# Kernel optimization log

Hardware: AMD Instinct MI355X
Metric: run time of the kernel (lower is better)

The kernel has to match this reference:

```python
import jax, jax.numpy as jnp
import numpy as np

NEG_INF = -1e30  # stand-in for float('-inf') that is fp16/bf16-safe


def setup_inputs() -> dict:
    key = jax.random.key(0)
    ks = jax.random.split(key, 6)
    B, S, D, E = 4, 4096, 2048, 64
    return {
        "x": jax.random.normal(ks[0], (B, S, D), dtype=jnp.float32),
        "router_w": jax.random.normal(ks[1], (E, D), dtype=jnp.float32) * (1.0 / np.sqrt(D)),
        "router_b": jax.random.normal(ks[2], (E,), dtype=jnp.float32) * 0.01,
        "noise_w": jax.random.normal(ks[3], (E, D), dtype=jnp.float32) * (1.0 / np.sqrt(D)),
        "noise_b": jax.random.normal(ks[4], (E,), dtype=jnp.float32) * 0.01,
        "noise_u": jax.random.uniform(ks[5], (B, S, E), dtype=jnp.float32),
        "top_k": 2,
    }


def reference(x, router_w, router_b, noise_w, noise_b, noise_u, top_k):
    E = router_w.shape[0]
    # dual linear projections: [B,S,D] x [D,E] -> [B,S,E]
    logits = jnp.einsum("bsd,ed->bse", x, router_w) + router_b
    noise_scale = jax.nn.softplus(jnp.einsum("bsd,ed->bse", x, noise_w) + noise_b)
    noisy = logits + noise_scale * noise_u  # noise_u plays role of torch.rand_like
    # top-k over experts
    max_k, max_k_index = jax.lax.top_k(noisy, top_k)  # [B,S,k]
    # scatter top-k values into -inf-filled tensor == keep noisy at topk slots
    keep = jnp.sum(jax.nn.one_hot(max_k_index, E, dtype=noisy.dtype), axis=-2) > 0  # [B,S,E]
    sparse = jnp.where(keep, noisy, NEG_INF)
    sf_sparse_topk = jax.nn.softmax(sparse, axis=-1)
    return (sf_sparse_topk, max_k_index)
```

## Files before the change

### kernel.cpp

```cpp
#include <hip/hip_runtime.h>
#include <math.h>

typedef __fp16   fp16x2  __attribute__((ext_vector_type(2)));
typedef _Float16 half8   __attribute__((ext_vector_type(8)));
typedef float    floatx4 __attribute__((ext_vector_type(4)));

#define M_TOTAL 16384
#define K_DIM   2048
#define NCOL    128
#define BM      32
#define BK      32
#define NT      256
#define NCHUNK  (K_DIM / BK)

#define A_HI  0
#define A_LO  1024
#define B_HI  2048
#define B_LO  6144
#define BUF_H 10240

__device__ __forceinline__ void gl_lds16(const _Float16* g, _Float16* l) {
    __builtin_amdgcn_global_load_lds((const __attribute__((address_space(1))) void*)g,
                                     (__attribute__((address_space(3))) void*)l, 16, 0, 0);
}

__device__ __forceinline__ void cvt_store(const float4 v, _Float16* hiP, _Float16* loP) {
    fp16x2 h01 = __builtin_amdgcn_cvt_pkrtz(v.x, v.y);
    fp16x2 h23 = __builtin_amdgcn_cvt_pkrtz(v.z, v.w);
    float r0 = (v.x - (float)h01.x) * 2048.0f;
    float r1 = (v.y - (float)h01.y) * 2048.0f;
    float r2 = (v.z - (float)h23.x) * 2048.0f;
    float r3 = (v.w - (float)h23.y) * 2048.0f;
    fp16x2 l01 = __builtin_amdgcn_cvt_pkrtz(r0, r1);
    fp16x2 l23 = __builtin_amdgcn_cvt_pkrtz(r2, r3);
    union { fp16x2 h[2]; uint2 u; } ph, pl;
    ph.h[0] = h01; ph.h[1] = h23;
    pl.h[0] = l01; pl.h[1] = l23;
    *(uint2*)hiP = ph.u;
    *(uint2*)loP = pl.u;
}

__global__ __launch_bounds__(256) void conv_w_kernel(
    const float* __restrict__ rw, const float* __restrict__ nw,
    _Float16* __restrict__ wsB)
{
    const int u   = blockIdx.x * 256 + threadIdx.x;
    const int col = u & 127;
    const int g   = (u >> 7) & 3;
    const int c   = u >> 9;
    const float* srcRow = (col < 64) ? (rw + (size_t)col * K_DIM)
                                     : (nw + (size_t)(col - 64) * K_DIM);
    const float* src = srcRow + c * BK + g * 8;
    const float4 v0 = *(const float4*)src;
    const float4 v1 = *(const float4*)(src + 4);
    union { fp16x2 h[4]; uint4 q; } ph, pl;
    ph.h[0] = __builtin_amdgcn_cvt_pkrtz(v0.x, v0.y);
    ph.h[1] = __builtin_amdgcn_cvt_pkrtz(v0.z, v0.w);
    ph.h[2] = __builtin_amdgcn_cvt_pkrtz(v1.x, v1.y);
    ph.h[3] = __builtin_amdgcn_cvt_pkrtz(v1.z, v1.w);
    pl.h[0] = __builtin_amdgcn_cvt_pkrtz((v0.x - (float)ph.h[0].x) * 2048.0f,
                                         (v0.y - (float)ph.h[0].y) * 2048.0f);
    pl.h[1] = __builtin_amdgcn_cvt_pkrtz((v0.z - (float)ph.h[1].x) * 2048.0f,
                                         (v0.w - (float)ph.h[1].y) * 2048.0f);
    pl.h[2] = __builtin_amdgcn_cvt_pkrtz((v1.x - (float)ph.h[2].x) * 2048.0f,
                                         (v1.y - (float)ph.h[2].y) * 2048.0f);
    pl.h[3] = __builtin_amdgcn_cvt_pkrtz((v1.z - (float)ph.h[3].x) * 2048.0f,
                                         (v1.w - (float)ph.h[3].y) * 2048.0f);
    const size_t base = (size_t)c * 8192 + ((size_t)g * 128 + col) * 8;
    *(uint4*)&wsB[base]        = ph.q;
    *(uint4*)&wsB[base + 4096] = pl.q;
}

__global__ __launch_bounds__(NT, 2) void gemm_router_kernel(
    const float* __restrict__ x,
    const _Float16* __restrict__ wsB,
    const float* __restrict__ router_b,
    const float* __restrict__ noise_b,
    const float* __restrict__ noise_u,
    float* __restrict__ out)
{
    __shared__ __align__(16) union {
        _Float16 S[2 * BUF_H];
        struct { float Cs[32][132]; float p1[32]; float p2[32]; int i1[32]; int i2[32]; } e;
    } sm;

    const int t    = threadIdx.x;
    const int lane = t & 63;
    const int w    = t >> 6;
    const int rowBase = blockIdx.x * BM;

    const int r = t >> 3, q = t & 7;
    const float* pa = x + (size_t)(rowBase + r) * K_DIM + q * 4;
    const int aw = ((q >> 1) * 32 + r) * 8 + (q & 1) * 4;

    const int lr  = lane & 15;
    const int lg4 = lane >> 4;
    const int mt0 = (w & 1) * 16;
    const int nt0 = (w >> 1) * 64;
    const int aOff = (lg4 * 32 + mt0 + lr) * 8;

    floatx4 acch[4], accx[4];
    #pragma unroll
    for (int ni = 0; ni < 4; ++ni) { acch[ni] = (floatx4)0.0f; accx[ni] = (floatx4)0.0f; }

    float4 aReg = *(const float4*)pa;
    {
        #pragma unroll
        for (int i = 0; i < 4; ++i) {
            const int n = w * 4 + i;
            gl_lds16(wsB + n * 512 + lane * 8, &sm.S[B_HI + n * 512]);
        }
    }
    cvt_store(aReg, &sm.S[A_HI + aw], &sm.S[A_LO + aw]);

    for (int c = 0; c < NCHUNK; ++c) {
        __syncthreads();
        _Float16* buf  = sm.S + (c & 1) * BUF_H;
        _Float16* bufn = sm.S + ((c + 1) & 1) * BUF_H;

        if (c + 1 < NCHUNK) {
            const _Float16* wc = wsB + (size_t)(c + 1) * 8192;
            #pragma unroll
            for (int i = 0; i < 4; ++i) {
                const int n = w * 4 + i;
                gl_lds16(wc + n * 512 + lane * 8, bufn + B_HI + n * 512);
            }
            aReg = *(const float4*)(pa + (c + 1) * BK);
        }

        const half8 ah = *(const half8*)&buf[A_HI + aOff];
        const half8 al = *(const half8*)&buf[A_LO + aOff];
        half8 bh[4], bl[4];
        #pragma unroll
        for (int ni = 0; ni < 4; ++ni) {
            const int bo = (lg4 * 128 + nt0 + ni * 16 + lr) * 8;
            bh[ni] = *(const half8*)&buf[B_HI + bo];
            bl[ni] = *(const half8*)&buf[B_LO + bo];
        }
        #pragma unroll
        for (int ni = 0; ni < 4; ++ni) {
            acch[ni] = __builtin_amdgcn_mfma_f32_16x16x32_f16(ah, bh[ni], acch[ni], 0, 0, 0);
            accx[ni] = __builtin_amdgcn_mfma_f32_16x16x32_f16(ah, bl[ni], accx[ni], 0, 0, 0);
            accx[ni] = __builtin_amdgcn_mfma_f32_16x16x32_f16(al, bh[ni], accx[ni], 0, 0, 0);
        }
        if (c + 1 < NCHUNK)
            cvt_store(aReg, &bufn[A_HI + aw], &bufn[A_LO + aw]);
    }

    #pragma unroll
    for (int ni = 0; ni < 4; ++ni) {
        const floatx4 v = acch[ni] + accx[ni] * (1.0f / 2048.0f);
        const int col = nt0 + ni * 16 + lr;
        #pragma unroll
        for (int reg = 0; reg < 4; ++reg)
            sm.e.Cs[mt0 + lg4 * 4 + reg][col] = v[reg];
    }
    __syncthreads();

    {
        const int sr = t >> 3;
        const int eg = (t & 7) * 8;
        const int grow = rowBase + sr;
        const float* urow = noise_u + (size_t)grow * 64 + eg;
        const float4 u0 = *(const float4*)urow;
        const float4 u1 = *(const float4*)(urow + 4);
        const float uu[8] = {u0.x, u0.y, u0.z, u0.w, u1.x, u1.y, u1.z, u1.w};
        float v1 = -3.0e38f, v2 = -3.0e38f;
        int i1 = 0, i2 = 0;
        #pragma unroll
        for (int j = 0; j < 8; ++j) {
            const int e = eg + j;
            const float lg = sm.e.Cs[sr][e] + router_b[e];
            const float nz = sm.e.Cs[sr][64 + e] + noise_b[e];
            const float sp = fmaxf(nz, 0.0f) + log1pf(expf(-fabsf(nz)));
            const float nv = lg + sp * uu[j];
            if (nv > v1)      { v2 = v1; i2 = i1; v1 = nv; i1 = e; }
            else if (nv > v2) { v2 = nv; i2 = e; }
        }
        #pragma unroll
        for (int m = 1; m < 8; m <<= 1) {
            const float ov1 = __shfl_xor(v1, m, 64);
            const int   oi1 = __shfl_xor(i1, m, 64);
            const float ov2 = __shfl_xor(v2, m, 64);
            const int   oi2 = __shfl_xor(i2, m, 64);
            const bool takeO = (ov1 > v1) || (ov1 == v1 && oi1 < i1);
            const float t1v = takeO ? ov1 : v1;  const int t1i = takeO ? oi1 : i1;
            const float c2v = takeO ? v1 : ov1;  const int c2i = takeO ? i1 : oi1;
            const float c3v = takeO ? ov2 : v2;  const int c3i = takeO ? oi2 : i2;
            const bool k2 = (c3v > c2v) || (c3v == c2v && c3i < c2i);
            v1 = t1v; i1 = t1i;
            v2 = k2 ? c3v : c2v; i2 = k2 ? c3i : c2i;
        }
        if ((t & 7) == 0) {
            const float e2 = expf(v2 - v1);
            const float dn = 1.0f + e2;
            sm.e.p1[sr] = 1.0f / dn;
            sm.e.p2[sr] = e2 / dn;
            sm.e.i1[sr] = i1;
            sm.e.i2[sr] = i2;
            float2 idx2;
            idx2.x = (float)i1;
            idx2.y = (float)i2;
            *(float2*)&out[(size_t)M_TOTAL * 64 + (size_t)grow * 2] = idx2;
        }
    }
    __syncthreads();

    {
        const int rr = t >> 3;
        const int e0 = (t & 7) * 8;
        const int g2 = rowBase + rr;
        const int j1 = sm.e.i1[rr], j2 = sm.e.i2[rr];
        const float q1 = sm.e.p1[rr], q2 = sm.e.p2[rr];
        float* orow = out + (size_t)g2 * 64;
        #pragma unroll
        for (int g = 0; g < 2; ++g) {
            const int b0 = e0 + g * 4;
            float4 v;
            v.x = (b0 + 0 == j1) ? q1 : (b0 + 0 == j2) ? q2 : 0.0f;
            v.y = (b0 + 1 == j1) ? q1 : (b0 + 1 == j2) ? q2 : 0.0f;
            v.z = (b0 + 2 == j1) ? q1 : (b0 + 2 == j2) ? q2 : 0.0f;
            v.w = (b0 + 3 == j1) ? q1 : (b0 + 3 == j2) ? q2 : 0.0f;
            *(float4*)&orow[b0] = v;
        }
    }
}

extern "C" void kernel_launch(void* const* d_in, const int* in_sizes, int n_in,
                              void* d_out, int out_size, void* d_ws, size_t ws_size,
                              hipStream_t stream) {
    const float* x  = (const float*)d_in[0];
    const float* rw = (const float*)d_in[1];
    const float* rb = (const float*)d_in[2];
    const float* nw = (const float*)d_in[3];
    const float* nb = (const float*)d_in[4];
    const float* nu = (const float*)d_in[5];
    float* out = (float*)d_out;
    _Float16* wsB = (_Float16*)d_ws;
    (void)in_sizes; (void)n_in; (void)out_size; (void)ws_size;

    hipLaunchKernelGGL(conv_w_kernel, dim3(128), dim3(256), 0, stream, rw, nw, wsB);
    hipLaunchKernelGGL(gemm_router_kernel, dim3(M_TOTAL / BM), dim3(NT), 0, stream,
                       x, wsB, rb, nb, nu, out);
}
```

Before: 239.7 us.

## Load A fragments directly to registers and make B LDS staging per-wave, barrier-free

Result: slower. 265.1 us (+10.6%).

```diff
diff --git a/kernel.cpp b/kernel.cpp
--- a/kernel.cpp
+++ b/kernel.cpp
@@ -7,37 +7,14 @@
 
 #define M_TOTAL 16384
 #define K_DIM   2048
-#define NCOL    128
 #define BM      32
 #define BK      32
 #define NT      256
 #define NCHUNK  (K_DIM / BK)
 
-#define A_HI  0
-#define A_LO  1024
-#define B_HI  2048
-#define B_LO  6144
-#define BUF_H 10240
-
 __device__ __forceinline__ void gl_lds16(const _Float16* g, _Float16* l) {
     __builtin_amdgcn_global_load_lds((const __attribute__((address_space(1))) void*)g,
                                      (__attribute__((address_space(3))) void*)l, 16, 0, 0);
-}
-
-__device__ __forceinline__ void cvt_store(const float4 v, _Float16* hiP, _Float16* loP) {
-    fp16x2 h01 = __builtin_amdgcn_cvt_pkrtz(v.x, v.y);
-    fp16x2 h23 = __builtin_amdgcn_cvt_pkrtz(v.z, v.w);
-    float r0 = (v.x - (float)h01.x) * 2048.0f;
-    float r1 = (v.y - (float)h01.y) * 2048.0f;
-    float r2 = (v.z - (float)h23.x) * 2048.0f;
-    float r3 = (v.w - (float)h23.y) * 2048.0f;
-    fp16x2 l01 = __builtin_amdgcn_cvt_pkrtz(r0, r1);
-    fp16x2 l23 = __builtin_amdgcn_cvt_pkrtz(r2, r3);
-    union { fp16x2 h[2]; uint2 u; } ph, pl;
-    ph.h[0] = h01; ph.h[1] = h23;
-    pl.h[0] = l01; pl.h[1] = l23;
-    *(uint2*)hiP = ph.u;
-    *(uint2*)loP = pl.u;
 }
 
 __global__ __launch_bounds__(256) void conv_w_kernel(
@@ -80,7 +57,7 @@
     float* __restrict__ out)
 {
     __shared__ __align__(16) union {
-        _Float16 S[2 * BUF_H];
+        _Float16 B[2][4][4096];
         struct { float Cs[32][132]; float p1[32]; float p2[32]; int i1[32]; int i2[32]; } e;
     } sm;
 
@@ -89,63 +66,87 @@
     const int w    = t >> 6;
     const int rowBase = blockIdx.x * BM;
 
-    const int r = t >> 3, q = t & 7;
-    const float* pa = x + (size_t)(rowBase + r) * K_DIM + q * 4;
-    const int aw = ((q >> 1) * 32 + r) * 8 + (q & 1) * 4;
-
     const int lr  = lane & 15;
     const int lg4 = lane >> 4;
     const int mt0 = (w & 1) * 16;
     const int nt0 = (w >> 1) * 64;
-    const int aOff = (lg4 * 32 + mt0 + lr) * 8;
+
+    const float* pa = x + (size_t)(rowBase + mt0 + lr) * K_DIM + lg4 * 8;
+    const _Float16* wsrc = wsB + (size_t)nt0 * 8 + (size_t)lane * 8;
+
+    _Float16* const b0 = &sm.B[0][w][0];
+    _Float16* const b1 = &sm.B[1][w][0];
+
+    #pragma unroll
+    for (int g = 0; g < 4; ++g) {
+        gl_lds16(wsrc + g * 1024,        b0 + g * 512);
+        gl_lds16(wsrc + 4096 + g * 1024, b0 + 2048 + g * 512);
+    }
+    float4 A0a = *(const float4*)(pa);
+    float4 A0b = *(const float4*)(pa + 4);
+    float4 A1a = *(const float4*)(pa + 32);
+    float4 A1b = *(const float4*)(pa + 36);
 
     floatx4 acch[4], accx[4];
     #pragma unroll
     for (int ni = 0; ni < 4; ++ni) { acch[ni] = (floatx4)0.0f; accx[ni] = (floatx4)0.0f; }
 
-    float4 aReg = *(const float4*)pa;
-    {
-        #pragma unroll
-        for (int i = 0; i < 4; ++i) {
-            const int n = w * 4 + i;
-            gl_lds16(wsB + n * 512 + lane * 8, &sm.S[B_HI + n * 512]);
-        }
-    }
-    cvt_store(aReg, &sm.S[A_HI + aw], &sm.S[A_LO + aw]);
-
+    #pragma unroll 2
     for (int c = 0; c < NCHUNK; ++c) {
-        __syncthreads();
-        _Float16* buf  = sm.S + (c & 1) * BUF_H;
-        _Float16* bufn = sm.S + ((c + 1) & 1) * BUF_H;
-
-        if (c + 1 < NCHUNK) {
-            const _Float16* wc = wsB + (size_t)(c + 1) * 8192;
-            #pragma unroll
-            for (int i = 0; i < 4; ++i) {
-                const int n = w * 4 + i;
-                gl_lds16(wc + n * 512 + lane * 8, bufn + B_HI + n * 512);
-            }
-            aReg = *(const float4*)(pa + (c + 1) * BK);
-        }
-
-        const half8 ah = *(const half8*)&buf[A_HI + aOff];
-        const half8 al = *(const half8*)&buf[A_LO + aOff];
+        _Float16* const cur = (c & 1) ? b1 : b0;
+        _Float16* const nxt = (c & 1) ? b0 : b1;
+
+        const int cn  = (c + 1 < NCHUNK) ? c + 1 : NCHUNK - 1;
+        const int cn2 = (c + 2 < NCHUNK) ? c + 2 : NCHUNK - 1;
+        const _Float16* wsn = wsrc + (size_t)cn * 8192;
+        #pragma unroll
+        for (int g = 0; g < 4; ++g) {
+            gl_lds16(wsn + g * 1024,        nxt + g * 512);
+            gl_lds16(wsn + 4096 + g * 1024, nxt + 2048 + g * 512);
+        }
+        const float4 A2a = *(const float4*)(pa + cn2 * 32);
+        const float4 A2b = *(const float4*)(pa + cn2 * 32 + 4);
+
+        asm volatile("s_waitcnt vmcnt(10)" ::: "memory");
+
         half8 bh[4], bl[4];
         #pragma unroll
         for (int ni = 0; ni < 4; ++ni) {
-            const int bo = (lg4 * 128 + nt0 + ni * 16 + lr) * 8;
-            bh[ni] = *(const half8*)&buf[B_HI + bo];
-            bl[ni] = *(const half8*)&buf[B_LO + bo];
-        }
+            const int co = lg4 * 512 + (ni * 16 + lr) * 8;
+            bh[ni] = *(const half8*)&cur[co];
+            bl[ni] = *(const half8*)&cur[2048 + co];
+        }
+
+        union { fp16x2 h[4]; half8 v; } H, L;
+        H.h[0] = __builtin_amdgcn_cvt_pkrtz(A0a.x, A0a.y);
+        H.h[1] = __builtin_amdgcn_cvt_pkrtz(A0a.z, A0a.w);
+        H.h[2] = __builtin_amdgcn_cvt_pkrtz(A0b.x, A0b.y);
+        H.h[3] = __builtin_amdgcn_cvt_pkrtz(A0b.z, A0b.w);
+        L.h[0] = __builtin_amdgcn_cvt_pkrtz((A0a.x - (float)H.h[0].x) * 2048.0f,
+                                            (A0a.y - (float)H.h[0].y) * 2048.0f);
+        L.h[1] = __builtin_amdgcn_cvt_pkrtz((A0a.z - (float)H.h[1].x) * 2048.0f,
+                                            (A0a.w - (float)H.h[1].y) * 2048.0f);
+        L.h[2] = __builtin_amdgcn_cvt_pkrtz((A0b.x - (float)H.h[2].x) * 2048.0f,
+                                            (A0b.y - (float)H.h[2].y) * 2048.0f);
+        L.h[3] = __builtin_amdgcn_cvt_pkrtz((A0b.z - (float)H.h[3].x) * 2048.0f,
+                                            (A0b.w - (float)H.h[3].y) * 2048.0f);
+        const half8 ah = H.v;
+        const half8 al = L.v;
+
+        __builtin_amdgcn_s_setprio(1);
         #pragma unroll
         for (int ni = 0; ni < 4; ++ni) {
             acch[ni] = __builtin_amdgcn_mfma_f32_16x16x32_f16(ah, bh[ni], acch[ni], 0, 0, 0);
             accx[ni] = __builtin_amdgcn_mfma_f32_16x16x32_f16(ah, bl[ni], accx[ni], 0, 0, 0);
             accx[ni] = __builtin_amdgcn_mfma_f32_16x16x32_f16(al, bh[ni], accx[ni], 0, 0, 0);
         }
-        if (c + 1 < NCHUNK)
-            cvt_store(aReg, &bufn[A_HI + aw], &bufn[A_LO + aw]);
-    }
+        __builtin_amdgcn_s_setprio(0);
+
+        A0a = A1a; A0b = A1b; A1a = A2a; A1b = A2b;
+    }
+
+    asm volatile("s_waitcnt vmcnt(0)" ::: "memory");
+    __syncthreads();
 
     #pragma unroll
     for (int ni = 0; ni < 4; ++ni) {
@@ -215,13 +216,13 @@
         float* orow = out + (size_t)g2 * 64;
         #pragma unroll
         for (int g = 0; g < 2; ++g) {
-            const int b0 = e0 + g * 4;
+            const int b0i = e0 + g * 4;
             float4 v;
-            v.x = (b0 + 0 == j1) ? q1 : (b0 + 0 == j2) ? q2 : 0.0f;
-            v.y = (b0 + 1 == j1) ? q1 : (b0 + 1 == j2) ? q2 : 0.0f;
-            v.z = (b0 + 2 == j1) ? q1 : (b0 + 2 == j2) ? q2 : 0.0f;
-            v.w = (b0 + 3 == j1) ? q1 : (b0 + 3 == j2) ? q2 : 0.0f;
-            *(float4*)&orow[b0] = v;
+            v.x = (b0i + 0 == j1) ? q1 : (b0i + 0 == j2) ? q2 : 0.0f;
+            v.y = (b0i + 1 == j1) ? q1 : (b0i + 1 == j2) ? q2 : 0.0f;
+            v.z = (b0i + 2 == j1) ? q1 : (b0i + 2 == j2) ? q2 : 0.0f;
+            v.w = (b0i + 3 == j1) ? q1 : (b0i + 3 == j2) ? q2 : 0.0f;
+            *(float4*)&orow[b0i] = v;
         }
     }
 }
```

## Triple-buffer LDS and deepen prefetch pipeline with manual waitcnt barriers

Applied to the files above, without the earlier changes.

Result: faster. 230.9 us (-3.7%).

```diff
diff --git a/kernel.cpp b/kernel.cpp
--- a/kernel.cpp
+++ b/kernel.cpp
@@ -80,7 +80,7 @@
     float* __restrict__ out)
 {
     __shared__ __align__(16) union {
-        _Float16 S[2 * BUF_H];
+        _Float16 S[3 * BUF_H];
         struct { float Cs[32][132]; float p1[32]; float p2[32]; int i1[32]; int i2[32]; } e;
     } sm;
 
@@ -103,49 +103,75 @@
     #pragma unroll
     for (int ni = 0; ni < 4; ++ni) { acch[ni] = (floatx4)0.0f; accx[ni] = (floatx4)0.0f; }
 
-    float4 aReg = *(const float4*)pa;
-    {
-        #pragma unroll
-        for (int i = 0; i < 4; ++i) {
-            const int n = w * 4 + i;
-            gl_lds16(wsB + n * 512 + lane * 8, &sm.S[B_HI + n * 512]);
-        }
-    }
-    cvt_store(aReg, &sm.S[A_HI + aw], &sm.S[A_LO + aw]);
+    _Float16* p0 = sm.S;
+    _Float16* p1 = sm.S + BUF_H;
+    _Float16* p2 = sm.S + 2 * BUF_H;
+
+    float4 a0v = *(const float4*)pa;
+    float4 a1v = *(const float4*)(pa + BK);
+    asm volatile("" ::: "memory");
+    float4 aS = *(const float4*)(pa + 2 * BK);
+    #pragma unroll
+    for (int i = 0; i < 4; ++i) {
+        const int n = w * 4 + i;
+        gl_lds16(wsB + n * 512 + lane * 8, p0 + B_HI + n * 512);
+    }
+    asm volatile("" ::: "memory");
+    float4 aN = *(const float4*)(pa + 3 * BK);
+    #pragma unroll
+    for (int i = 0; i < 4; ++i) {
+        const int n = w * 4 + i;
+        gl_lds16(wsB + 8192 + n * 512 + lane * 8, p1 + B_HI + n * 512);
+    }
+    asm volatile("" ::: "memory");
+    asm volatile("s_waitcnt vmcnt(10)" ::: "memory");
+    cvt_store(a0v, &p0[A_HI + aw], &p0[A_LO + aw]);
+    cvt_store(a1v, &p1[A_HI + aw], &p1[A_LO + aw]);
+    asm volatile("s_waitcnt lgkmcnt(0)" ::: "memory");
 
     for (int c = 0; c < NCHUNK; ++c) {
-        __syncthreads();
-        _Float16* buf  = sm.S + (c & 1) * BUF_H;
-        _Float16* bufn = sm.S + ((c + 1) & 1) * BUF_H;
-
-        if (c + 1 < NCHUNK) {
-            const _Float16* wc = wsB + (size_t)(c + 1) * 8192;
+        asm volatile("s_waitcnt vmcnt(5)" ::: "memory");
+        asm volatile("s_barrier" ::: "memory");
+
+        const int cn2 = (c + 2 < NCHUNK) ? c + 2 : NCHUNK - 1;
+        const int cn4 = (c + 4 < NCHUNK) ? c + 4 : NCHUNK - 1;
+        float4 aNew = *(const float4*)(pa + cn4 * BK);
+        {
+            const _Float16* wc = wsB + (size_t)cn2 * 8192;
             #pragma unroll
             for (int i = 0; i < 4; ++i) {
                 const int n = w * 4 + i;
-                gl_lds16(wc + n * 512 + lane * 8, bufn + B_HI + n * 512);
+                gl_lds16(wc + n * 512 + lane * 8, p2 + B_HI + n * 512);
             }
-            aReg = *(const float4*)(pa + (c + 1) * BK);
-        }
-
-        const half8 ah = *(const half8*)&buf[A_HI + aOff];
-        const half8 al = *(const half8*)&buf[A_LO + aOff];
+        }
+
+        const half8 ah = *(const half8*)&p0[A_HI + aOff];
+        const half8 al = *(const half8*)&p0[A_LO + aOff];
         half8 bh[4], bl[4];
         #pragma unroll
         for (int ni = 0; ni < 4; ++ni) {
             const int bo = (lg4 * 128 + nt0 + ni * 16 + lr) * 8;
-            bh[ni] = *(const half8*)&buf[B_HI + bo];
-            bl[ni] = *(const half8*)&buf[B_LO + bo];
-        }
+            bh[ni] = *(const half8*)&p0[B_HI + bo];
+            bl[ni] = *(const half8*)&p0[B_LO + bo];
+        }
+
+        __builtin_amdgcn_s_setprio(1);
         #pragma unroll
         for (int ni = 0; ni < 4; ++ni) {
             acch[ni] = __builtin_amdgcn_mfma_f32_16x16x32_f16(ah, bh[ni], acch[ni], 0, 0, 0);
             accx[ni] = __builtin_amdgcn_mfma_f32_16x16x32_f16(ah, bl[ni], accx[ni], 0, 0, 0);
             accx[ni] = __builtin_amdgcn_mfma_f32_16x16x32_f16(al, bh[ni], accx[ni], 0, 0, 0);
         }
-        if (c + 1 < NCHUNK)
-            cvt_store(aReg, &bufn[A_HI + aw], &bufn[A_LO + aw]);
-    }
+        __builtin_amdgcn_s_setprio(0);
+
+        cvt_store(aS, &p2[A_HI + aw], &p2[A_LO + aw]);
+        aS = aN; aN = aNew;
+
+        _Float16* tmp = p0; p0 = p1; p1 = p2; p2 = tmp;
+    }
+
+    asm volatile("s_waitcnt vmcnt(0)" ::: "memory");
+    __syncthreads();
 
     #pragma unroll
     for (int ni = 0; ni < 4; ++ni) {
```

## Halve GEMM row tile to 16 rows and retarget occupancy to four blocks per CU

Applied to the files above, without the earlier changes.

New measurement: 256.0 us. +6.8%, slower.

```diff
diff --git a/kernel.cpp b/kernel.cpp
--- a/kernel.cpp
+++ b/kernel.cpp
@@ -8,36 +8,31 @@
 #define M_TOTAL 16384
 #define K_DIM   2048
 #define NCOL    128
-#define BM      32
+#define BM      16
 #define BK      32
 #define NT      256
 #define NCHUNK  (K_DIM / BK)
 
 #define A_HI  0
-#define A_LO  1024
-#define B_HI  2048
-#define B_LO  6144
-#define BUF_H 10240
+#define A_LO  512
+#define B_HI  1024
+#define B_LO  5120
+#define BUF_H 9216
 
 __device__ __forceinline__ void gl_lds16(const _Float16* g, _Float16* l) {
     __builtin_amdgcn_global_load_lds((const __attribute__((address_space(1))) void*)g,
                                      (__attribute__((address_space(3))) void*)l, 16, 0, 0);
 }
 
-__device__ __forceinline__ void cvt_store(const float4 v, _Float16* hiP, _Float16* loP) {
-    fp16x2 h01 = __builtin_amdgcn_cvt_pkrtz(v.x, v.y);
-    fp16x2 h23 = __builtin_amdgcn_cvt_pkrtz(v.z, v.w);
-    float r0 = (v.x - (float)h01.x) * 2048.0f;
-    float r1 = (v.y - (float)h01.y) * 2048.0f;
-    float r2 = (v.z - (float)h23.x) * 2048.0f;
-    float r3 = (v.w - (float)h23.y) * 2048.0f;
-    fp16x2 l01 = __builtin_amdgcn_cvt_pkrtz(r0, r1);
-    fp16x2 l23 = __builtin_amdgcn_cvt_pkrtz(r2, r3);
-    union { fp16x2 h[2]; uint2 u; } ph, pl;
-    ph.h[0] = h01; ph.h[1] = h23;
-    pl.h[0] = l01; pl.h[1] = l23;
-    *(uint2*)hiP = ph.u;
-    *(uint2*)loP = pl.u;
+__device__ __forceinline__ void cvt_store2(const float2 v, _Float16* hiP, _Float16* loP) {
+    fp16x2 h = __builtin_amdgcn_cvt_pkrtz(v.x, v.y);
+    float r0 = (v.x - (float)h.x) * 2048.0f;
+    float r1 = (v.y - (float)h.y) * 2048.0f;
+    fp16x2 l = __builtin_amdgcn_cvt_pkrtz(r0, r1);
+    union { fp16x2 h2; unsigned u; } ph, pl;
+    ph.h2 = h; pl.h2 = l;
+    *(unsigned*)hiP = ph.u;
+    *(unsigned*)loP = pl.u;
 }
 
 __global__ __launch_bounds__(256) void conv_w_kernel(
@@ -71,7 +66,7 @@
     *(uint4*)&wsB[base + 4096] = pl.q;
 }
 
-__global__ __launch_bounds__(NT, 2) void gemm_router_kernel(
+__global__ __launch_bounds__(NT, 4) void gemm_router_kernel(
     const float* __restrict__ x,
     const _Float16* __restrict__ wsB,
     const float* __restrict__ router_b,
@@ -81,7 +76,7 @@
 {
     __shared__ __align__(16) union {
         _Float16 S[2 * BUF_H];
-        struct { float Cs[32][132]; float p1[32]; float p2[32]; int i1[32]; int i2[32]; } e;
+        struct { float Cs[16][132]; float p1[16]; float p2[16]; int i1[16]; int i2[16]; } e;
     } sm;
 
     const int t    = threadIdx.x;
@@ -89,21 +84,19 @@
     const int w    = t >> 6;
     const int rowBase = blockIdx.x * BM;
 
-    const int r = t >> 3, q = t & 7;
-    const float* pa = x + (size_t)(rowBase + r) * K_DIM + q * 4;
-    const int aw = ((q >> 1) * 32 + r) * 8 + (q & 1) * 4;
+    const int rr = t >> 4, q2 = t & 15;
+    const float* pa = x + (size_t)(rowBase + rr) * K_DIM + q2 * 2;
+    const int aw = (((q2 >> 2) * 16 + rr) * 8) + ((q2 & 3) * 2);
 
     const int lr  = lane & 15;
     const int lg4 = lane >> 4;
-    const int mt0 = (w & 1) * 16;
-    const int nt0 = (w >> 1) * 64;
-    const int aOff = (lg4 * 32 + mt0 + lr) * 8;
-
-    floatx4 acch[4], accx[4];
+    const int nt0 = w * 32;
+    const int aOff = (lg4 * 16 + lr) * 8;
+
+    floatx4 acch[2], accx[2];
     #pragma unroll
-    for (int ni = 0; ni < 4; ++ni) { acch[ni] = (floatx4)0.0f; accx[ni] = (floatx4)0.0f; }
-
-    float4 aReg = *(const float4*)pa;
+    for (int ni = 0; ni < 2; ++ni) { acch[ni] = (floatx4)0.0f; accx[ni] = (floatx4)0.0f; }
+
     {
         #pragma unroll
         for (int i = 0; i < 4; ++i) {
@@ -111,13 +104,17 @@
             gl_lds16(wsB + n * 512 + lane * 8, &sm.S[B_HI + n * 512]);
         }
     }
-    cvt_store(aReg, &sm.S[A_HI + aw], &sm.S[A_LO + aw]);
+    {
+        const float2 a0 = *(const float2*)pa;
+        cvt_store2(a0, &sm.S[A_HI + aw], &sm.S[A_LO + aw]);
+    }
 
     for (int c = 0; c < NCHUNK; ++c) {
         __syncthreads();
         _Float16* buf  = sm.S + (c & 1) * BUF_H;
         _Float16* bufn = sm.S + ((c + 1) & 1) * BUF_H;
 
+        float2 aReg;
         if (c + 1 < NCHUNK) {
             const _Float16* wc = wsB + (size_t)(c + 1) * 8192;
             #pragma unroll
@@ -125,39 +122,39 @@
                 const int n = w * 4 + i;
                 gl_lds16(wc + n * 512 + lane * 8, bufn + B_HI + n * 512);
             }
-            aReg = *(const float4*)(pa + (c + 1) * BK);
+            aReg = *(const float2*)(pa + (c + 1) * BK);
         }
 
         const half8 ah = *(const half8*)&buf[A_HI + aOff];
         const half8 al = *(const half8*)&buf[A_LO + aOff];
-        half8 bh[4], bl[4];
-        #pragma unroll
-        for (int ni = 0; ni < 4; ++ni) {
+        half8 bh[2], bl[2];
+        #pragma unroll
+        for (int ni = 0; ni < 2; ++ni) {
             const int bo = (lg4 * 128 + nt0 + ni * 16 + lr) * 8;
             bh[ni] = *(const half8*)&buf[B_HI + bo];
             bl[ni] = *(const half8*)&buf[B_LO + bo];
         }
         #pragma unroll
-        for (int ni = 0; ni < 4; ++ni) {
+        for (int ni = 0; ni < 2; ++ni) {
             acch[ni] = __builtin_amdgcn_mfma_f32_16x16x32_f16(ah, bh[ni], acch[ni], 0, 0, 0);
             accx[ni] = __builtin_amdgcn_mfma_f32_16x16x32_f16(ah, bl[ni], accx[ni], 0, 0, 0);
             accx[ni] = __builtin_amdgcn_mfma_f32_16x16x32_f16(al, bh[ni], accx[ni], 0, 0, 0);
         }
         if (c + 1 < NCHUNK)
-            cvt_store(aReg, &bufn[A_HI + aw], &bufn[A_LO + aw]);
+            cvt_store2(aReg, &bufn[A_HI + aw], &bufn[A_LO + aw]);
     }
 
     #pragma unroll
-    for (int ni = 0; ni < 4; ++ni) {
+    for (int ni = 0; ni < 2; ++ni) {
         const floatx4 v = acch[ni] + accx[ni] * (1.0f / 2048.0f);
         const int col = nt0 + ni * 16 + lr;
         #pragma unroll
         for (int reg = 0; reg < 4; ++reg)
-            sm.e.Cs[mt0 + lg4 * 4 + reg][col] = v[reg];
+            sm.e.Cs[lg4 * 4 + reg][col] = v[reg];
     }
     __syncthreads();
 
-    {
+    if (t < 128) {
         const int sr = t >> 3;
         const int eg = (t & 7) * 8;
         const int grow = rowBase + sr;
@@ -206,21 +203,21 @@
     }
     __syncthreads();
 
-    {
-        const int rr = t >> 3;
+    if (t < 128) {
+        const int r2 = t >> 3;
         const int e0 = (t & 7) * 8;
-        const int g2 = rowBase + rr;
-        const int j1 = sm.e.i1[rr], j2 = sm.e.i2[rr];
-        const float q1 = sm.e.p1[rr], q2 = sm.e.p2[rr];
+        const int g2 = rowBase + r2;
+        const int j1 = sm.e.i1[r2], j2 = sm.e.i2[r2];
+        const float q1 = sm.e.p1[r2], q2v = sm.e.p2[r2];
         float* orow = out + (size_t)g2 * 64;
         #pragma unroll
         for (int g = 0; g < 2; ++g) {
             const int b0 = e0 + g * 4;
             float4 v;
-            v.x = (b0 + 0 == j1) ? q1 : (b0 + 0 == j2) ? q2 : 0.0f;
-            v.y = (b0 + 1 == j1) ? q1 : (b0 + 1 == j2) ? q2 : 0.0f;
-            v.z = (b0 + 2 == j1) ? q1 : (b0 + 2 == j2) ? q2 : 0.0f;
-            v.w = (b0 + 3 == j1) ? q1 : (b0 + 3 == j2) ? q2 : 0.0f;
+            v.x = (b0 + 0 == j1) ? q1 : (b0 + 0 == j2) ? q2v : 0.0f;
+            v.y = (b0 + 1 == j1) ? q1 : (b0 + 1 == j2) ? q2v : 0.0f;
+            v.z = (b0 + 2 == j1) ? q1 : (b0 + 2 == j2) ? q2v : 0.0f;
+            v.w = (b0 + 3 == j1) ? q1 : (b0 + 3 == j2) ? q2v : 0.0f;
             *(float4*)&orow[b0] = v;
         }
     }
```
